# Kernel tuning notes

Hardware: AMD Instinct MI355X
Metric: run time of the kernel (lower is better)

Reference implementation:

```python
import jax, jax.numpy as jnp
import numpy as np

CHEB_K = 3

def avwgcn(x, E, w_pool, b_pool):
    # x: [B,N,C], E: [N,D], w_pool: [D,K,C,O], b_pool: [D,O]
    N = E.shape[0]
    supports = jax.nn.softmax(jax.nn.relu(E @ E.T), axis=1)  # [N,N]
    slist = [jnp.eye(N, dtype=x.dtype), supports]
    for _ in range(CHEB_K - 2):
        slist.append(2.0 * supports @ slist[-1] - slist[-2])
    S = jnp.stack(slist)                         # [K,N,N]
    W = jnp.einsum('nd,dkio->nkio', E, w_pool)   # [N,K,C,O]
    b = E @ b_pool                               # [N,O]
    xg = jnp.einsum('knm,bmc->bnkc', S, x)       # [B,N,K,C]
    return jnp.einsum('bnki,nkio->bno', xg, W) + b


def setup_inputs() -> dict:
    key = jax.random.key(0)
    ks = jax.random.split(key, 9)
    B, N, C_IN, C_OUT, D = 16, 2048, 64, 64, 10
    x = jax.random.normal(ks[0], (B, N, C_IN), dtype=jnp.float32)
    state = jax.random.normal(ks[1], (B, N, C_OUT), dtype=jnp.float32)
    node_embeddings = jax.random.normal(ks[2], (N, D), dtype=jnp.float32)
    gate_wpool = jax.random.normal(ks[3], (D, CHEB_K, C_IN + C_OUT, 2 * C_OUT), dtype=jnp.float32) * 0.1
    gate_bpool = jax.random.normal(ks[4], (D, 2 * C_OUT), dtype=jnp.float32) * 0.1
    upd_wpool = jax.random.normal(ks[5], (D, CHEB_K, C_IN + C_OUT, C_OUT), dtype=jnp.float32) * 0.1
    upd_bpool = jax.random.normal(ks[6], (D, C_OUT), dtype=jnp.float32) * 0.1
    lin_w = jax.random.normal(ks[7], (64, 128), dtype=jnp.float32) * 0.1
    lin_b = jax.random.normal(ks[8], (64,), dtype=jnp.float32) * 0.1
    return {"x": x, "state": state, "node_embeddings": node_embeddings,
            "gate_wpool": gate_wpool, "gate_bpool": gate_bpool,
            "upd_wpool": upd_wpool, "upd_bpool": upd_bpool,
            "lin_w": lin_w, "lin_b": lin_b}


def reference(x, state, node_embeddings, gate_wpool, gate_bpool, upd_wpool, upd_bpool, lin_w, lin_b):
    input_and_state = jnp.concatenate([x, state], axis=-1)          # [B,N,128]
    z_r = jax.nn.sigmoid(avwgcn(input_and_state, node_embeddings, gate_wpool, gate_bpool))  # [B,N,128]
    z_r = z_r @ lin_w.T + lin_b                                     # [B,N,64]
    candidate = jnp.concatenate([x, z_r], axis=-1)                  # [B,N,128]
    hc = jnp.tanh(avwgcn(candidate, node_embeddings, upd_wpool, upd_bpool))  # [B,N,64]
    return hc
```

## Files before the change

### kernel.cpp

```cpp
#include <hip/hip_runtime.h>

typedef unsigned short u16;
typedef short s16x8 __attribute__((ext_vector_type(8)));
typedef _Float16 h16x8 __attribute__((ext_vector_type(8)));
typedef float f32x4 __attribute__((ext_vector_type(4)));
typedef u16 u16x4 __attribute__((ext_vector_type(4)));

#define DEV static __device__ __forceinline__

DEV u16 f2h(float x){ union { _Float16 h; u16 u; } v; v.h = (_Float16)x; return v.u; }
DEV float h2f(u16 u){ union { u16 u; _Float16 h; } v; v.u = u; return (float)v.h; }
DEV void split_h(float x, u16& h, u16& l){
    h = f2h(x);
    l = f2h(x - h2f(h));
}
DEV h16x8 H8(s16x8 v){ union { s16x8 s; h16x8 h; } u; u.s = v; return u.h; }
DEV f32x4 mfma16(s16x8 a, s16x8 b, f32x4 c){
    return __builtin_amdgcn_mfma_f32_16x16x32_f16(H8(a), H8(b), c, 0, 0, 0);
}

DEV int swz(int r, int m){ return (m & ~0x38) | ((((m >> 3) ^ r) & 7) << 3); }

DEV void gll16(const u16* g, u16* l){
    __builtin_amdgcn_global_load_lds((const __attribute__((address_space(1))) void*)g,
                                     (__attribute__((address_space(3))) void*)l, 16, 0, 0);
}

__global__ __launch_bounds__(256) void k_supports(const float* __restrict__ E,
                                                  u16* __restrict__ Sh, u16* __restrict__ Sl)
{
    const int n = blockIdx.x, tid = threadIdx.x;
    const int w = tid >> 6, lane = tid & 63;
    __shared__ float red[8];

    float en[10];
    #pragma unroll
    for (int d = 0; d < 10; d++) en[d] = E[n*10 + d];

    float v[8];
    #pragma unroll
    for (int i = 0; i < 8; i++){
        int m = tid + i*256;
        const float* em = E + m*10;
        float s = 0.f;
        #pragma unroll
        for (int d = 0; d < 10; d++) s += en[d]*em[d];
        v[i] = fmaxf(s, 0.f);
    }
    float mx = v[0];
    #pragma unroll
    for (int i = 1; i < 8; i++) mx = fmaxf(mx, v[i]);
    #pragma unroll
    for (int off = 32; off > 0; off >>= 1) mx = fmaxf(mx, __shfl_xor(mx, off));
    if (lane == 0) red[w] = mx;
    __syncthreads();
    mx = fmaxf(fmaxf(red[0], red[1]), fmaxf(red[2], red[3]));
    __syncthreads();

    float sum = 0.f;
    #pragma unroll
    for (int i = 0; i < 8; i++){ v[i] = __expf(v[i] - mx); sum += v[i]; }
    #pragma unroll
    for (int off = 32; off > 0; off >>= 1) sum += __shfl_xor(sum, off);
    if (lane == 0) red[4 + w] = sum;
    __syncthreads();
    sum = red[4] + red[5] + red[6] + red[7];
    float inv = 1.f / sum;

    #pragma unroll
    for (int i = 0; i < 8; i++){
        float p = v[i] * inv;
        u16 h, l; split_h(p, h, l);
        int m = tid + i*256;
        int ms = swz(n, m);
        Sh[n*2048 + ms] = h;
        Sl[n*2048 + ms] = l;
    }
}

__global__ __launch_bounds__(256) void k_prep(const float* __restrict__ E,
    const float* __restrict__ gwp, const float* __restrict__ gbp,
    const float* __restrict__ uwp, const float* __restrict__ ubp,
    const float* __restrict__ x,   const float* __restrict__ state,
    const float* __restrict__ lw,
    u16* __restrict__ wg, u16* __restrict__ wu,
    float* __restrict__ bg, float* __restrict__ bu,
    u16* __restrict__ xt, u16* __restrict__ lwt)
{
    long idx = (long)blockIdx.x*256 + threadIdx.x;
    if (idx < 491520){
        int kk = (int)(idx & 31);
        int o  = (int)((idx >> 5) & 127);
        int r2 = (int)(idx >> 12);
        int d = r2 % 10, jc = r2 / 10;
        int j = jc*32 + kk;
        int k = j >> 7, i = j & 127;
        float v = gwp[(((d*3 + k)*128) + i)*128 + o];
        wg[idx] = f2h(v);
    } else if (idx < 737280){
        long t = idx - 491520;
        int kk = (int)(t & 31);
        int o  = (int)((t >> 5) & 63);
        int r2 = (int)(t >> 11);
        int d = r2 % 10, jc = r2 / 10;
        int j = jc*32 + kk;
        int k = j >> 7, i = j & 127;
        float v = uwp[(((d*3 + k)*128) + i)*64 + o];
        wu[t] = f2h(v);
    } else if (idx < 999424){
        long t = idx - 737280; int n = (int)(t >> 7), o = (int)(t & 127);
        float s = 0.f;
        #pragma unroll
        for (int d = 0; d < 10; d++) s += E[n*10+d]*gbp[d*128+o];
        bg[t] = s;
    } else if (idx < 1130496){
        long t = idx - 999424; int n = (int)(t >> 6), o = (int)(t & 63);
        float s = 0.f;
        #pragma unroll
        for (int d = 0; d < 10; d++) s += E[n*10+d]*ubp[d*64+o];
        bu[t] = s;
    } else if (idx < 5324800){
        long t = idx - 1130496;
        int colG = (int)(t >> 11), m = (int)(t & 2047);
        int b = colG >> 7, c = colG & 127;
        float v = (c < 64) ? x[((long)(b*2048)+m)*64 + c]
                           : state[((long)(b*2048)+m)*64 + c - 64];
        xt[(long)colG*2048 + swz(colG, m)] = f2h(v);
    } else if (idx < 5332992){
        long t = idx - 5324800;
        lwt[t] = f2h(lw[t]);
    }
}

template<int EPI>
__global__ __launch_bounds__(256) void k_gemm(
    const u16* __restrict__ Ah, const u16* __restrict__ Al,
    const u16* __restrict__ Bt,
    u16* __restrict__ Ot, float* __restrict__ Orow,
    const u16* __restrict__ Xt)
{
    __shared__ __attribute__((aligned(16))) u16 AsH[2][64*64];
    __shared__ __attribute__((aligned(16))) u16 AsL[2][64*64];
    __shared__ __attribute__((aligned(16))) u16 Bs[2][128*64];
    const int tid = threadIdx.x;
    const int xc = blockIdx.x & 7, ii = blockIdx.x >> 3;
    const int bm = ((xc & 3)*8 + (ii & 7)) << 6;
    const int bn = ((xc >> 2)*8 + (ii >> 3)) << 7;
    const int w = tid >> 6, lane = tid & 63;
    const int wm = (w & 1) << 5;
    const int wn = (w >> 1) << 6;
    const int lr = lane & 15, lk = lane >> 4;

    const int srow = tid >> 3, scol = (tid & 7) << 3;
    const long a0 = (long)(bm + srow)*2048 + scol;
    const long a1 = a0 + 32*2048;
    const long b0 = (long)(bn + srow)*2048 + scol;
    const long b1 = b0 + 32*2048;
    const long b2 = b0 + 64*2048;
    const long b3 = b0 + 96*2048;
    const int l0 = tid*8, l1 = tid*8 + 2048;

    const int c0 = (lk ^ (lr & 7)) << 3;
    const int c1 = c0 ^ 32;

#define STAGE(B, K) do { \
        gll16(Ah + a0 + (K), &AsH[B][l0]); \
        gll16(Ah + a1 + (K), &AsH[B][l1]); \
        gll16(Al + a0 + (K), &AsL[B][l0]); \
        gll16(Al + a1 + (K), &AsL[B][l1]); \
        gll16(Bt + b0 + (K), &Bs[B][l0]); \
        gll16(Bt + b1 + (K), &Bs[B][l1]); \
        gll16(Bt + b2 + (K), &Bs[B][l0 + 4096]); \
        gll16(Bt + b3 + (K), &Bs[B][l1 + 4096]); \
    } while(0)

    f32x4 acc[2][4];
    const f32x4 Z4 = {0.f, 0.f, 0.f, 0.f};
    #pragma unroll
    for (int i = 0; i < 2; i++)
        #pragma unroll
        for (int j = 0; j < 4; j++) acc[i][j] = Z4;

    STAGE(0, 0);
    __syncthreads();
    int cur = 0;
    for (int k0 = 0; k0 < 2048; k0 += 64){
        if (k0 + 64 < 2048) STAGE(cur ^ 1, k0 + 64);
        const u16* ah = AsH[cur];
        const u16* al = AsL[cur];
        const u16* bs = Bs[cur];
        #pragma unroll
        for (int s2 = 0; s2 < 2; s2++){
            const int cc = s2 ? c1 : c0;
            s16x8 bfv[4], af[2];
            #pragma unroll
            for (int ni = 0; ni < 4; ni++)
                bfv[ni] = *(const s16x8*)&bs[(wn + ni*16 + lr)*64 + cc];
            #pragma unroll
            for (int mi = 0; mi < 2; mi++)
                af[mi] = *(const s16x8*)&ah[(wm + mi*16 + lr)*64 + cc];
            #pragma unroll
            for (int mi = 0; mi < 2; mi++)
                #pragma unroll
                for (int ni = 0; ni < 4; ni++)
                    acc[mi][ni] = mfma16(af[mi], bfv[ni], acc[mi][ni]);
            #pragma unroll
            for (int mi = 0; mi < 2; mi++)
                af[mi] = *(const s16x8*)&al[(wm + mi*16 + lr)*64 + cc];
            #pragma unroll
            for (int mi = 0; mi < 2; mi++)
                #pragma unroll
                for (int ni = 0; ni < 4; ni++)
                    acc[mi][ni] = mfma16(af[mi], bfv[ni], acc[mi][ni]);
        }
        __syncthreads();
        cur ^= 1;
    }
#undef STAGE

    #pragma unroll
    for (int mi = 0; mi < 2; mi++){
        #pragma unroll
        for (int ni = 0; ni < 4; ni++){
            int i0 = bm + wm + mi*16 + lk*4;
            int j  = bn + wn + ni*16 + lr;
            f32x4 v = acc[mi][ni];
            if constexpr (EPI){
                u16x4 xh = *(const u16x4*)(Xt + (long)j*2048 + swz(j, i0));
                #pragma unroll
                for (int r = 0; r < 4; r++)
                    v[r] = 2.f*v[r] - h2f(xh[r]);
            }
            int bb = j >> 7, cc = j & 127;
            float* rp = Orow + ((long)bb*2048 + i0)*128 + cc;
            #pragma unroll
            for (int r = 0; r < 4; r++) rp[(long)r*128] = v[r];
            if constexpr (!EPI){
                u16x4 oh;
                #pragma unroll
                for (int r = 0; r < 4; r++) oh[r] = f2h(v[r]);
                *(u16x4*)(Ot + (long)j*2048 + swz(j, i0)) = oh;
            }
        }
    }
}

template<int OFULL, int ACT, int FUSE>
__global__ __launch_bounds__(256, 2) void k_combine(
    const float* __restrict__ G1r, const float* __restrict__ G2r,
    const float* __restrict__ x, const float* __restrict__ second,
    const u16* __restrict__ W,
    const float* __restrict__ bias, const float* __restrict__ E,
    float* __restrict__ out, u16* __restrict__ XtT,
    const u16* __restrict__ lwt, const float* __restrict__ lb)
{
    constexpr int NO = OFULL/32;
    __shared__ u16 Ash[64*40], Asl[64*40];
    __shared__ float Et[640];
    __shared__ u16 Zh[FUSE ? 64*136 : 1];
    __shared__ u16 Zl[FUSE ? 64*136 : 1];
    const int tid = threadIdx.x, bid = blockIdx.x;
    const int b = bid >> 5, n0 = (bid & 31) << 6;
    const int w = tid >> 6, lane = tid & 63;
    const int wm = (w & 1)*32, wo = (w >> 1)*(OFULL/2);
    const int lr = lane & 15, lk = lane >> 4;

    for (int i = tid; i < 640; i += 256)
        Et[i] = E[(n0 + (i & 63))*10 + (i >> 6)];

    const f32x4 Z4 = {0.f, 0.f, 0.f, 0.f};
    f32x4 acc[2][NO];
    #pragma unroll
    for (int mi = 0; mi < 2; mi++)
        #pragma unroll
        for (int oi = 0; oi < NO; oi++) acc[mi][oi] = Z4;

    const long rowbase = (long)b*2048 + n0;
    const int laneoff = (wo + lr)*32 + lk*8;

    s16x8 pbh[3][NO];

    for (int jc = 0; jc < 12; jc++){
        {
            const long t0 = (long)(jc*10 + 0)*OFULL*32;
            const long t1 = (long)(jc*10 + 1)*OFULL*32;
            #pragma unroll
            for (int oi = 0; oi < NO; oi++){
                pbh[0][oi] = *(const s16x8*)(W + t0 + laneoff + oi*16*32);
                pbh[1][oi] = *(const s16x8*)(W + t1 + laneoff + oi*16*32);
            }
        }
        __syncthreads();
        {
            const float* src; int stride;
            if (jc < 4){
                int col0 = jc*32;
                src = (col0 < 64) ? (x + rowbase*64 + col0)
                                  : (second + rowbase*64 + (col0 - 64));
                stride = 64;
            } else if (jc < 8){
                src = G1r + rowbase*128 + (jc-4)*32; stride = 128;
            } else {
                src = G2r + rowbase*128 + (jc-8)*32; stride = 128;
            }
            int row = tid >> 2, c8 = (tid & 3)*8;
            f32x4 s0 = *(const f32x4*)(src + (long)row*stride + c8);
            f32x4 s1 = *(const f32x4*)(src + (long)row*stride + c8 + 4);
            s16x8 vh, vl;
            #pragma unroll
            for (int t = 0; t < 4; t++){
                u16 h,l; split_h(s0[t], h, l); vh[t]=(short)h; vl[t]=(short)l;
            }
            #pragma unroll
            for (int t = 0; t < 4; t++){
                u16 h,l; split_h(s1[t], h, l); vh[4+t]=(short)h; vl[4+t]=(short)l;
            }
            *(s16x8*)&Ash[row*40 + c8] = vh;
            *(s16x8*)&Asl[row*40 + c8] = vl;
        }
        __syncthreads();

        s16x8 ah[2], al[2];
        #pragma unroll
        for (int mi = 0; mi < 2; mi++){
            ah[mi] = *(const s16x8*)&Ash[(wm + mi*16 + lr)*40 + lk*8];
            al[mi] = *(const s16x8*)&Asl[(wm + mi*16 + lr)*40 + lk*8];
        }

        #pragma unroll
        for (int d = 0; d < 10; d++){
            const int cur = d % 3;
            if (d < 8){
                const int nx = (d + 2) % 3;
                const long t2 = (long)(jc*10 + d + 2)*OFULL*32;
                #pragma unroll
                for (int oi = 0; oi < NO; oi++)
                    pbh[nx][oi] = *(const s16x8*)(W + t2 + laneoff + oi*16*32);
            }
            f32x4 Cd[2][NO];
            #pragma unroll
            for (int mi = 0; mi < 2; mi++)
                #pragma unroll
                for (int oi = 0; oi < NO; oi++)
                    Cd[mi][oi] = mfma16(ah[mi], pbh[cur][oi], Z4);
            #pragma unroll
            for (int mi = 0; mi < 2; mi++)
                #pragma unroll
                for (int oi = 0; oi < NO; oi++)
                    Cd[mi][oi] = mfma16(al[mi], pbh[cur][oi], Cd[mi][oi]);
            #pragma unroll
            for (int mi = 0; mi < 2; mi++){
                f32x4 e4 = *(const f32x4*)&Et[d*64 + wm + mi*16 + lk*4];
                #pragma unroll
                for (int oi = 0; oi < NO; oi++) acc[mi][oi] += e4 * Cd[mi][oi];
            }
        }
    }

    if constexpr (!FUSE){
        #pragma unroll
        for (int mi = 0; mi < 2; mi++){
            #pragma unroll
            for (int oi = 0; oi < NO; oi++){
                int mrow = n0 + wm + mi*16 + lk*4;
                int o = wo + oi*16 + lr;
                #pragma unroll
                for (int r = 0; r < 4; r++){
                    float v = acc[mi][oi][r] + bias[(long)(mrow + r)*OFULL + o];
                    v = (ACT == 0) ? (1.f/(1.f + __expf(-v))) : tanhf(v);
                    out[((long)b*2048 + mrow + r)*OFULL + o] = v;
                }
            }
        }
    } else {
        #pragma unroll
        for (int mi = 0; mi < 2; mi++){
            #pragma unroll
            for (int oi = 0; oi < NO; oi++){
                int lrow = wm + mi*16 + lk*4;
                int o = wo + oi*16 + lr;
                #pragma unroll
                for (int r = 0; r < 4; r++){
                    float v = acc[mi][oi][r] + bias[(long)(n0 + lrow + r)*OFULL + o];
                    v = 1.f/(1.f + __expf(-v));
                    u16 h, l; split_h(v, h, l);
                    Zh[(lrow + r)*136 + o] = h;
                    Zl[(lrow + r)*136 + o] = l;
                }
            }
        }
        __syncthreads();
        f32x4 az[4];
        #pragma unroll
        for (int mi = 0; mi < 4; mi++) az[mi] = Z4;
        const int oz = w*16 + lr;
        #pragma unroll
        for (int ks = 0; ks < 4; ks++){
            s16x8 bw = *(const s16x8*)(lwt + oz*128 + ks*32 + lk*8);
            #pragma unroll
            for (int mi = 0; mi < 4; mi++){
                s16x8 zh = *(const s16x8*)&Zh[(mi*16 + lr)*136 + ks*32 + lk*8];
                az[mi] = mfma16(zh, bw, az[mi]);
            }
            #pragma unroll
            for (int mi = 0; mi < 4; mi++){
                s16x8 zl = *(const s16x8*)&Zl[(mi*16 + lr)*136 + ks*32 + lk*8];
                az[mi] = mfma16(zl, bw, az[mi]);
            }
        }
        const float lbv = lb[w*16 + lr];
        const int colG = b*128 + 64 + w*16 + lr;
        #pragma unroll
        for (int mi = 0; mi < 4; mi++){
            int mrow = n0 + mi*16 + lk*4;
            u16x4 tq;
            #pragma unroll
            for (int r = 0; r < 4; r++){
                float v = az[mi][r] + lbv;
                out[((long)b*2048 + mrow + r)*64 + w*16 + lr] = v;
                tq[r] = f2h(v);
            }
            *(u16x4*)(XtT + (long)colG*2048 + swz(colG, mrow)) = tq;
        }
    }
}

extern "C" void kernel_launch(void* const* d_in, const int* in_sizes, int n_in,
                              void* d_out, int out_size, void* d_ws, size_t ws_size,
                              hipStream_t stream)
{
    const float* x   = (const float*)d_in[0];
    const float* st  = (const float*)d_in[1];
    const float* E   = (const float*)d_in[2];
    const float* gwp = (const float*)d_in[3];
    const float* gbp = (const float*)d_in[4];
    const float* uwp = (const float*)d_in[5];
    const float* ubp = (const float*)d_in[6];
    const float* lw  = (const float*)d_in[7];
    const float* lb  = (const float*)d_in[8];
    float* out = (float*)d_out;
    char* ws = (char*)d_ws;

    const size_t MB8 = 8388608;
    u16*   Sh   = (u16*)(ws);
    u16*   Sl   = (u16*)(ws + 1*MB8);
    u16*   Xt   = (u16*)(ws + 2*MB8);
    u16*   G1t  = (u16*)(ws + 3*MB8);
    float* G1row= (float*)(ws + 4*MB8);
    float* G2row= (float*)(ws + 6*MB8);
    float* zr   = (float*)(ws + 8*MB8);
    char*  p    = ws + 9*MB8;
    u16* wg = (u16*)p;             p += 983040;
    u16* wu = (u16*)p;             p += 491520;
    float* bg = (float*)p;         p += 1048576;
    float* bu = (float*)p;         p += 524288;
    u16* lwt = (u16*)p;            p += 16384;

    k_supports<<<dim3(2048), dim3(256), 0, stream>>>(E, Sh, Sl);
    k_prep<<<dim3(20832), dim3(256), 0, stream>>>(E, gwp, gbp, uwp, ubp, x, st, lw,
                                                  wg, wu, bg, bu, Xt, lwt);
    k_gemm<0><<<dim3(512), dim3(256), 0, stream>>>(Sh, Sl, Xt, G1t, G1row,
                                                   (const u16*)nullptr);
    k_gemm<1><<<dim3(512), dim3(256), 0, stream>>>(Sh, Sl, G1t, (u16*)nullptr, G2row,
                                                   Xt);
    k_combine<128,0,1><<<dim3(512), dim3(256), 0, stream>>>(G1row, G2row, x, st,
                                                            wg, bg, E, zr, Xt, lwt, lb);
    k_gemm<0><<<dim3(512), dim3(256), 0, stream>>>(Sh, Sl, Xt, G1t, G1row,
                                                   (const u16*)nullptr);
    k_gemm<1><<<dim3(512), dim3(256), 0, stream>>>(Sh, Sl, G1t, (u16*)nullptr, G2row,
                                                   Xt);
    k_combine<64,1,0><<<dim3(512), dim3(256), 0, stream>>>(G1row, G2row, x, zr,
                                                           wu, bu, E, out,
                                                           (u16*)nullptr,
                                                           (const u16*)nullptr,
                                                           (const float*)nullptr);
}
```

Before: 357.3 us.

## Switch GEMM to 32x32x16 MFMA and fold supports kernel into prep

Replaces the 16x16x32 MFMA tiling in the propagation GEMM with 32x32x16 MFMAs: each wave now computes two 32x32 tiles, with the LDS fragment addressing and epilogue register mapping rewritten to match. This cuts the number of LDS fragment reads per MFMA and the instruction count. Separately, the softmax-supports kernel is merged into the prep kernel as its first 2048 blocks, saving one launch. The new swizzled read index and output mapping must line up exactly with the existing swizzle, which is a correctness risk.

```diff
diff --git a/kernel.cpp b/kernel.cpp
--- a/kernel.cpp
+++ b/kernel.cpp
@@ -4,6 +4,7 @@
 typedef short s16x8 __attribute__((ext_vector_type(8)));
 typedef _Float16 h16x8 __attribute__((ext_vector_type(8)));
 typedef float f32x4 __attribute__((ext_vector_type(4)));
+typedef float f32x16 __attribute__((ext_vector_type(16)));
 typedef u16 u16x4 __attribute__((ext_vector_type(4)));
 
 #define DEV static __device__ __forceinline__
@@ -18,64 +19,15 @@
 DEV f32x4 mfma16(s16x8 a, s16x8 b, f32x4 c){
     return __builtin_amdgcn_mfma_f32_16x16x32_f16(H8(a), H8(b), c, 0, 0, 0);
 }
+DEV f32x16 mfma32(s16x8 a, s16x8 b, f32x16 c){
+    return __builtin_amdgcn_mfma_f32_32x32x16_f16(H8(a), H8(b), c, 0, 0, 0);
+}
 
 DEV int swz(int r, int m){ return (m & ~0x38) | ((((m >> 3) ^ r) & 7) << 3); }
 
 DEV void gll16(const u16* g, u16* l){
     __builtin_amdgcn_global_load_lds((const __attribute__((address_space(1))) void*)g,
                                      (__attribute__((address_space(3))) void*)l, 16, 0, 0);
-}
-
-__global__ __launch_bounds__(256) void k_supports(const float* __restrict__ E,
-                                                  u16* __restrict__ Sh, u16* __restrict__ Sl)
-{
-    const int n = blockIdx.x, tid = threadIdx.x;
-    const int w = tid >> 6, lane = tid & 63;
-    __shared__ float red[8];
-
-    float en[10];
-    #pragma unroll
-    for (int d = 0; d < 10; d++) en[d] = E[n*10 + d];
-
-    float v[8];
-    #pragma unroll
-    for (int i = 0; i < 8; i++){
-        int m = tid + i*256;
-        const float* em = E + m*10;
-        float s = 0.f;
-        #pragma unroll
-        for (int d = 0; d < 10; d++) s += en[d]*em[d];
-        v[i] = fmaxf(s, 0.f);
-    }
-    float mx = v[0];
-    #pragma unroll
-    for (int i = 1; i < 8; i++) mx = fmaxf(mx, v[i]);
-    #pragma unroll
-    for (int off = 32; off > 0; off >>= 1) mx = fmaxf(mx, __shfl_xor(mx, off));
-    if (lane == 0) red[w] = mx;
-    __syncthreads();
-    mx = fmaxf(fmaxf(red[0], red[1]), fmaxf(red[2], red[3]));
-    __syncthreads();
-
-    float sum = 0.f;
-    #pragma unroll
-    for (int i = 0; i < 8; i++){ v[i] = __expf(v[i] - mx); sum += v[i]; }
-    #pragma unroll
-    for (int off = 32; off > 0; off >>= 1) sum += __shfl_xor(sum, off);
-    if (lane == 0) red[4 + w] = sum;
-    __syncthreads();
-    sum = red[4] + red[5] + red[6] + red[7];
-    float inv = 1.f / sum;
-
-    #pragma unroll
-    for (int i = 0; i < 8; i++){
-        float p = v[i] * inv;
-        u16 h, l; split_h(p, h, l);
-        int m = tid + i*256;
-        int ms = swz(n, m);
-        Sh[n*2048 + ms] = h;
-        Sl[n*2048 + ms] = l;
-    }
 }
 
 __global__ __launch_bounds__(256) void k_prep(const float* __restrict__ E,
@@ -85,9 +37,56 @@
     const float* __restrict__ lw,
     u16* __restrict__ wg, u16* __restrict__ wu,
     float* __restrict__ bg, float* __restrict__ bu,
-    u16* __restrict__ xt, u16* __restrict__ lwt)
+    u16* __restrict__ xt, u16* __restrict__ lwt,
+    u16* __restrict__ Sh, u16* __restrict__ Sl)
 {
-    long idx = (long)blockIdx.x*256 + threadIdx.x;
+    __shared__ float red[8];
+    const int tid = threadIdx.x;
+    if (blockIdx.x < 2048){
+        const int n = blockIdx.x;
+        const int w = tid >> 6, lane = tid & 63;
+        float en[10];
+        #pragma unroll
+        for (int d = 0; d < 10; d++) en[d] = E[n*10 + d];
+        float v[8];
+        #pragma unroll
+        for (int i = 0; i < 8; i++){
+            int m = tid + i*256;
+            const float* em = E + m*10;
+            float s = 0.f;
+            #pragma unroll
+            for (int d = 0; d < 10; d++) s += en[d]*em[d];
+            v[i] = fmaxf(s, 0.f);
+        }
+        float mx = v[0];
+        #pragma unroll
+        for (int i = 1; i < 8; i++) mx = fmaxf(mx, v[i]);
+        #pragma unroll
+        for (int off = 32; off > 0; off >>= 1) mx = fmaxf(mx, __shfl_xor(mx, off));
+        if (lane == 0) red[w] = mx;
+        __syncthreads();
+        mx = fmaxf(fmaxf(red[0], red[1]), fmaxf(red[2], red[3]));
+        __syncthreads();
+        float sum = 0.f;
+        #pragma unroll
+        for (int i = 0; i < 8; i++){ v[i] = __expf(v[i] - mx); sum += v[i]; }
+        #pragma unroll
+        for (int off = 32; off > 0; off >>= 1) sum += __shfl_xor(sum, off);
+        if (lane == 0) red[4 + w] = sum;
+        __syncthreads();
+        sum = red[4] + red[5] + red[6] + red[7];
+        float inv = 1.f / sum;
+        #pragma unroll
+        for (int i = 0; i < 8; i++){
+            float p = v[i] * inv;
+            u16 h, l; split_h(p, h, l);
+            int ms = swz(n, tid + i*256);
+            Sh[n*2048 + ms] = h;
+            Sl[n*2048 + ms] = l;
+        }
+        return;
+    }
+    long idx = (long)(blockIdx.x - 2048)*256 + tid;
     if (idx < 491520){
         int kk = (int)(idx & 31);
         int o  = (int)((idx >> 5) & 127);
@@ -149,7 +148,9 @@
     const int w = tid >> 6, lane = tid & 63;
     const int wm = (w & 1) << 5;
     const int wn = (w >> 1) << 6;
-    const int lr = lane & 15, lk = lane >> 4;
+    const int r31 = lane & 31;
+    const int hk  = lane >> 5;
+    const int key = lane & 7;
 
     const int srow = tid >> 3, scol = (tid & 7) << 3;
     const long a0 = (long)(bm + srow)*2048 + scol;
@@ -159,9 +160,6 @@
     const long b2 = b0 + 64*2048;
     const long b3 = b0 + 96*2048;
     const int l0 = tid*8, l1 = tid*8 + 2048;
-
-    const int c0 = (lk ^ (lr & 7)) << 3;
-    const int c1 = c0 ^ 32;
 
 #define STAGE(B, K) do { \
         gll16(Ah + a0 + (K), &AsH[B][l0]); \
@@ -174,12 +172,11 @@
         gll16(Bt + b3 + (K), &Bs[B][l1 + 4096]); \
     } while(0)
 
-    f32x4 acc[2][4];
-    const f32x4 Z4 = {0.f, 0.f, 0.f, 0.f};
+    f32x16 acc[2];
     #pragma unroll
     for (int i = 0; i < 2; i++)
         #pragma unroll
-        for (int j = 0; j < 4; j++) acc[i][j] = Z4;
+        for (int r = 0; r < 16; r++) acc[i][r] = 0.f;
 
     STAGE(0, 0);
     __syncthreads();
@@ -190,28 +187,16 @@
         const u16* al = AsL[cur];
         const u16* bs = Bs[cur];
         #pragma unroll
-        for (int s2 = 0; s2 < 2; s2++){
-            const int cc = s2 ? c1 : c0;
-            s16x8 bfv[4], af[2];
-            #pragma unroll
-            for (int ni = 0; ni < 4; ni++)
-                bfv[ni] = *(const s16x8*)&bs[(wn + ni*16 + lr)*64 + cc];
-            #pragma unroll
-            for (int mi = 0; mi < 2; mi++)
-                af[mi] = *(const s16x8*)&ah[(wm + mi*16 + lr)*64 + cc];
-            #pragma unroll
-            for (int mi = 0; mi < 2; mi++)
-                #pragma unroll
-                for (int ni = 0; ni < 4; ni++)
-                    acc[mi][ni] = mfma16(af[mi], bfv[ni], acc[mi][ni]);
-            #pragma unroll
-            for (int mi = 0; mi < 2; mi++)
-                af[mi] = *(const s16x8*)&al[(wm + mi*16 + lr)*64 + cc];
-            #pragma unroll
-            for (int mi = 0; mi < 2; mi++)
-                #pragma unroll
-                for (int ni = 0; ni < 4; ni++)
-                    acc[mi][ni] = mfma16(af[mi], bfv[ni], acc[mi][ni]);
+        for (int ks = 0; ks < 4; ks++){
+            const int ca = (((2*ks + hk) ^ key)) << 3;
+            s16x8 bv0 = *(const s16x8*)&bs[(wn +  0 + r31)*64 + ca];
+            s16x8 bv1 = *(const s16x8*)&bs[(wn + 32 + r31)*64 + ca];
+            s16x8 avh = *(const s16x8*)&ah[(wm + r31)*64 + ca];
+            acc[0] = mfma32(avh, bv0, acc[0]);
+            acc[1] = mfma32(avh, bv1, acc[1]);
+            s16x8 avl = *(const s16x8*)&al[(wm + r31)*64 + ca];
+            acc[0] = mfma32(avl, bv0, acc[0]);
+            acc[1] = mfma32(avl, bv1, acc[1]);
         }
         __syncthreads();
         cur ^= 1;
@@ -219,26 +204,28 @@
 #undef STAGE
 
     #pragma unroll
-    for (int mi = 0; mi < 2; mi++){
-        #pragma unroll
-        for (int ni = 0; ni < 4; ni++){
-            int i0 = bm + wm + mi*16 + lk*4;
-            int j  = bn + wn + ni*16 + lr;
-            f32x4 v = acc[mi][ni];
+    for (int ni = 0; ni < 2; ni++){
+        int j  = bn + wn + ni*32 + r31;
+        int bb = j >> 7, cc = j & 127;
+        #pragma unroll
+        for (int g = 0; g < 4; g++){
+            int i0 = bm + wm + 4*hk + 8*g;
+            f32x4 v;
+            #pragma unroll
+            for (int q = 0; q < 4; q++) v[q] = acc[ni][4*g + q];
             if constexpr (EPI){
                 u16x4 xh = *(const u16x4*)(Xt + (long)j*2048 + swz(j, i0));
                 #pragma unroll
-                for (int r = 0; r < 4; r++)
-                    v[r] = 2.f*v[r] - h2f(xh[r]);
-            }
-            int bb = j >> 7, cc = j & 127;
+                for (int q = 0; q < 4; q++)
+                    v[q] = 2.f*v[q] - h2f(xh[q]);
+            }
             float* rp = Orow + ((long)bb*2048 + i0)*128 + cc;
             #pragma unroll
-            for (int r = 0; r < 4; r++) rp[(long)r*128] = v[r];
+            for (int q = 0; q < 4; q++) rp[(long)q*128] = v[q];
             if constexpr (!EPI){
                 u16x4 oh;
                 #pragma unroll
-                for (int r = 0; r < 4; r++) oh[r] = f2h(v[r]);
+                for (int q = 0; q < 4; q++) oh[q] = f2h(v[q]);
                 *(u16x4*)(Ot + (long)j*2048 + swz(j, i0)) = oh;
             }
         }
@@ -456,9 +443,8 @@
     float* bu = (float*)p;         p += 524288;
     u16* lwt = (u16*)p;            p += 16384;
 
-    k_supports<<<dim3(2048), dim3(256), 0, stream>>>(E, Sh, Sl);
-    k_prep<<<dim3(20832), dim3(256), 0, stream>>>(E, gwp, gbp, uwp, ubp, x, st, lw,
-                                                  wg, wu, bg, bu, Xt, lwt);
+    k_prep<<<dim3(22880), dim3(256), 0, stream>>>(E, gwp, gbp, uwp, ubp, x, st, lw,
+                                                  wg, wu, bg, bu, Xt, lwt, Sh, Sl);
     k_gemm<0><<<dim3(512), dim3(256), 0, stream>>>(Sh, Sl, Xt, G1t, G1row,
                                                    (const u16*)nullptr);
     k_gemm<1><<<dim3(512), dim3(256), 0, stream>>>(Sh, Sl, G1t, (u16*)nullptr, G2row,
```

Result: slower. 374.1 us (+4.7%).

## Merge supports into prep kernel and widen gate combine to 512 threads

Applied to the files above, without the earlier changes.

The softmax-supports kernel is folded into the prep kernel as its first 2048 blocks, which removes one launch and lets the two independent pieces of work overlap. The gate combine kernel becomes a dedicated 512-thread version in which each of eight waves owns 16 output columns across all 64 rows, so per-thread register pressure drops and more waves are available to hide latency. The fused z_r linear stage is split across the eight waves by rows and columns. The cost is more redundant A-tile fragment loads per wave and different occupancy behaviour at the larger block size.

```diff
diff --git a/kernel.cpp b/kernel.cpp
--- a/kernel.cpp
+++ b/kernel.cpp
@@ -24,58 +24,6 @@
 DEV void gll16(const u16* g, u16* l){
     __builtin_amdgcn_global_load_lds((const __attribute__((address_space(1))) void*)g,
                                      (__attribute__((address_space(3))) void*)l, 16, 0, 0);
-}
-
-__global__ __launch_bounds__(256) void k_supports(const float* __restrict__ E,
-                                                  u16* __restrict__ Sh, u16* __restrict__ Sl)
-{
-    const int n = blockIdx.x, tid = threadIdx.x;
-    const int w = tid >> 6, lane = tid & 63;
-    __shared__ float red[8];
-
-    float en[10];
-    #pragma unroll
-    for (int d = 0; d < 10; d++) en[d] = E[n*10 + d];
-
-    float v[8];
-    #pragma unroll
-    for (int i = 0; i < 8; i++){
-        int m = tid + i*256;
-        const float* em = E + m*10;
-        float s = 0.f;
-        #pragma unroll
-        for (int d = 0; d < 10; d++) s += en[d]*em[d];
-        v[i] = fmaxf(s, 0.f);
-    }
-    float mx = v[0];
-    #pragma unroll
-    for (int i = 1; i < 8; i++) mx = fmaxf(mx, v[i]);
-    #pragma unroll
-    for (int off = 32; off > 0; off >>= 1) mx = fmaxf(mx, __shfl_xor(mx, off));
-    if (lane == 0) red[w] = mx;
-    __syncthreads();
-    mx = fmaxf(fmaxf(red[0], red[1]), fmaxf(red[2], red[3]));
-    __syncthreads();
-
-    float sum = 0.f;
-    #pragma unroll
-    for (int i = 0; i < 8; i++){ v[i] = __expf(v[i] - mx); sum += v[i]; }
-    #pragma unroll
-    for (int off = 32; off > 0; off >>= 1) sum += __shfl_xor(sum, off);
-    if (lane == 0) red[4 + w] = sum;
-    __syncthreads();
-    sum = red[4] + red[5] + red[6] + red[7];
-    float inv = 1.f / sum;
-
-    #pragma unroll
-    for (int i = 0; i < 8; i++){
-        float p = v[i] * inv;
-        u16 h, l; split_h(p, h, l);
-        int m = tid + i*256;
-        int ms = swz(n, m);
-        Sh[n*2048 + ms] = h;
-        Sl[n*2048 + ms] = l;
-    }
 }
 
 __global__ __launch_bounds__(256) void k_prep(const float* __restrict__ E,
@@ -85,9 +33,56 @@
     const float* __restrict__ lw,
     u16* __restrict__ wg, u16* __restrict__ wu,
     float* __restrict__ bg, float* __restrict__ bu,
-    u16* __restrict__ xt, u16* __restrict__ lwt)
+    u16* __restrict__ xt, u16* __restrict__ lwt,
+    u16* __restrict__ Sh, u16* __restrict__ Sl)
 {
-    long idx = (long)blockIdx.x*256 + threadIdx.x;
+    __shared__ float red[8];
+    const int tid = threadIdx.x;
+    if (blockIdx.x < 2048){
+        const int n = blockIdx.x;
+        const int w = tid >> 6, lane = tid & 63;
+        float en[10];
+        #pragma unroll
+        for (int d = 0; d < 10; d++) en[d] = E[n*10 + d];
+        float v[8];
+        #pragma unroll
+        for (int i = 0; i < 8; i++){
+            int m = tid + i*256;
+            const float* em = E + m*10;
+            float s = 0.f;
+            #pragma unroll
+            for (int d = 0; d < 10; d++) s += en[d]*em[d];
+            v[i] = fmaxf(s, 0.f);
+        }
+        float mx = v[0];
+        #pragma unroll
+        for (int i = 1; i < 8; i++) mx = fmaxf(mx, v[i]);
+        #pragma unroll
+        for (int off = 32; off > 0; off >>= 1) mx = fmaxf(mx, __shfl_xor(mx, off));
+        if (lane == 0) red[w] = mx;
+        __syncthreads();
+        mx = fmaxf(fmaxf(red[0], red[1]), fmaxf(red[2], red[3]));
+        __syncthreads();
+        float sum = 0.f;
+        #pragma unroll
+        for (int i = 0; i < 8; i++){ v[i] = __expf(v[i] - mx); sum += v[i]; }
+        #pragma unroll
+        for (int off = 32; off > 0; off >>= 1) sum += __shfl_xor(sum, off);
+        if (lane == 0) red[4 + w] = sum;
+        __syncthreads();
+        sum = red[4] + red[5] + red[6] + red[7];
+        float inv = 1.f / sum;
+        #pragma unroll
+        for (int i = 0; i < 8; i++){
+            float p = v[i] * inv;
+            u16 h, l; split_h(p, h, l);
+            int ms = swz(n, tid + i*256);
+            Sh[n*2048 + ms] = h;
+            Sl[n*2048 + ms] = l;
+        }
+        return;
+    }
+    long idx = (long)(blockIdx.x - 2048)*256 + tid;
     if (idx < 491520){
         int kk = (int)(idx & 31);
         int o  = (int)((idx >> 5) & 127);
@@ -245,8 +240,7 @@
     }
 }
 
-template<int OFULL, int ACT, int FUSE>
-__global__ __launch_bounds__(256, 2) void k_combine(
+__global__ __launch_bounds__(512) void k_combineG(
     const float* __restrict__ G1r, const float* __restrict__ G2r,
     const float* __restrict__ x, const float* __restrict__ second,
     const u16* __restrict__ W,
@@ -254,41 +248,34 @@
     float* __restrict__ out, u16* __restrict__ XtT,
     const u16* __restrict__ lwt, const float* __restrict__ lb)
 {
-    constexpr int NO = OFULL/32;
     __shared__ u16 Ash[64*40], Asl[64*40];
     __shared__ float Et[640];
-    __shared__ u16 Zh[FUSE ? 64*136 : 1];
-    __shared__ u16 Zl[FUSE ? 64*136 : 1];
+    __shared__ u16 Zh[64*136], Zl[64*136];
     const int tid = threadIdx.x, bid = blockIdx.x;
     const int b = bid >> 5, n0 = (bid & 31) << 6;
     const int w = tid >> 6, lane = tid & 63;
-    const int wm = (w & 1)*32, wo = (w >> 1)*(OFULL/2);
+    const int wo = w << 4;
     const int lr = lane & 15, lk = lane >> 4;
 
-    for (int i = tid; i < 640; i += 256)
+    for (int i = tid; i < 640; i += 512)
         Et[i] = E[(n0 + (i & 63))*10 + (i >> 6)];
 
     const f32x4 Z4 = {0.f, 0.f, 0.f, 0.f};
-    f32x4 acc[2][NO];
-    #pragma unroll
-    for (int mi = 0; mi < 2; mi++)
-        #pragma unroll
-        for (int oi = 0; oi < NO; oi++) acc[mi][oi] = Z4;
+    f32x4 acc[4];
+    #pragma unroll
+    for (int mi = 0; mi < 4; mi++) acc[mi] = Z4;
 
     const long rowbase = (long)b*2048 + n0;
     const int laneoff = (wo + lr)*32 + lk*8;
 
-    s16x8 pbh[3][NO];
+    s16x8 pbh[3];
 
     for (int jc = 0; jc < 12; jc++){
         {
-            const long t0 = (long)(jc*10 + 0)*OFULL*32;
-            const long t1 = (long)(jc*10 + 1)*OFULL*32;
-            #pragma unroll
-            for (int oi = 0; oi < NO; oi++){
-                pbh[0][oi] = *(const s16x8*)(W + t0 + laneoff + oi*16*32);
-                pbh[1][oi] = *(const s16x8*)(W + t1 + laneoff + oi*16*32);
-            }
+            const long t0 = (long)(jc*10 + 0)*128*32;
+            const long t1 = (long)(jc*10 + 1)*128*32;
+            pbh[0] = *(const s16x8*)(W + t0 + laneoff);
+            pbh[1] = *(const s16x8*)(W + t1 + laneoff);
         }
         __syncthreads();
         {
@@ -303,6 +290,150 @@
             } else {
                 src = G2r + rowbase*128 + (jc-8)*32; stride = 128;
             }
+            int row = tid >> 3, c4 = (tid & 7)*4;
+            f32x4 s0 = *(const f32x4*)(src + (long)row*stride + c4);
+            u16x4 vh, vl;
+            #pragma unroll
+            for (int t = 0; t < 4; t++){
+                u16 h,l; split_h(s0[t], h, l); vh[t]=h; vl[t]=l;
+            }
+            *(u16x4*)&Ash[row*40 + c4] = vh;
+            *(u16x4*)&Asl[row*40 + c4] = vl;
+        }
+        __syncthreads();
+
+        s16x8 ah[4], al[4];
+        #pragma unroll
+        for (int mi = 0; mi < 4; mi++){
+            ah[mi] = *(const s16x8*)&Ash[(mi*16 + lr)*40 + lk*8];
+            al[mi] = *(const s16x8*)&Asl[(mi*16 + lr)*40 + lk*8];
+        }
+
+        #pragma unroll
+        for (int d = 0; d < 10; d++){
+            const int cur = d % 3;
+            if (d < 8){
+                const int nx = (d + 2) % 3;
+                const long t2 = (long)(jc*10 + d + 2)*128*32;
+                pbh[nx] = *(const s16x8*)(W + t2 + laneoff);
+            }
+            f32x4 Cd[4];
+            #pragma unroll
+            for (int mi = 0; mi < 4; mi++)
+                Cd[mi] = mfma16(ah[mi], pbh[cur], Z4);
+            #pragma unroll
+            for (int mi = 0; mi < 4; mi++)
+                Cd[mi] = mfma16(al[mi], pbh[cur], Cd[mi]);
+            #pragma unroll
+            for (int mi = 0; mi < 4; mi++){
+                f32x4 e4 = *(const f32x4*)&Et[d*64 + mi*16 + lk*4];
+                acc[mi] += e4 * Cd[mi];
+            }
+        }
+    }
+
+    #pragma unroll
+    for (int mi = 0; mi < 4; mi++){
+        int lrow = mi*16 + lk*4;
+        int o = wo + lr;
+        #pragma unroll
+        for (int r = 0; r < 4; r++){
+            float v = acc[mi][r] + bias[(long)(n0 + lrow + r)*128 + o];
+            v = 1.f/(1.f + __expf(-v));
+            u16 h, l; split_h(v, h, l);
+            Zh[(lrow + r)*136 + o] = h;
+            Zl[(lrow + r)*136 + o] = l;
+        }
+    }
+    __syncthreads();
+    f32x4 az[2] = {Z4, Z4};
+    const int ow = (w & 3) << 4;
+    const int rh = (w >> 2) << 5;
+    #pragma unroll
+    for (int ks = 0; ks < 4; ks++){
+        s16x8 bw = *(const s16x8*)(lwt + (ow + lr)*128 + ks*32 + lk*8);
+        #pragma unroll
+        for (int mi = 0; mi < 2; mi++){
+            s16x8 zh = *(const s16x8*)&Zh[(rh + mi*16 + lr)*136 + ks*32 + lk*8];
+            az[mi] = mfma16(zh, bw, az[mi]);
+        }
+        #pragma unroll
+        for (int mi = 0; mi < 2; mi++){
+            s16x8 zl = *(const s16x8*)&Zl[(rh + mi*16 + lr)*136 + ks*32 + lk*8];
+            az[mi] = mfma16(zl, bw, az[mi]);
+        }
+    }
+    const float lbv = lb[ow + lr];
+    const int colG = b*128 + 64 + ow + lr;
+    #pragma unroll
+    for (int mi = 0; mi < 2; mi++){
+        int mrow = n0 + rh + mi*16 + lk*4;
+        u16x4 tq;
+        #pragma unroll
+        for (int r = 0; r < 4; r++){
+            float v = az[mi][r] + lbv;
+            out[((long)b*2048 + mrow + r)*64 + ow + lr] = v;
+            tq[r] = f2h(v);
+        }
+        *(u16x4*)(XtT + (long)colG*2048 + swz(colG, mrow)) = tq;
+    }
+}
+
+template<int OFULL, int ACT>
+__global__ __launch_bounds__(256, 2) void k_combine(
+    const float* __restrict__ G1r, const float* __restrict__ G2r,
+    const float* __restrict__ x, const float* __restrict__ second,
+    const u16* __restrict__ W,
+    const float* __restrict__ bias, const float* __restrict__ E,
+    float* __restrict__ out)
+{
+    constexpr int NO = OFULL/32;
+    __shared__ u16 Ash[64*40], Asl[64*40];
+    __shared__ float Et[640];
+    const int tid = threadIdx.x, bid = blockIdx.x;
+    const int b = bid >> 5, n0 = (bid & 31) << 6;
+    const int w = tid >> 6, lane = tid & 63;
+    const int wm = (w & 1)*32, wo = (w >> 1)*(OFULL/2);
+    const int lr = lane & 15, lk = lane >> 4;
+
+    for (int i = tid; i < 640; i += 256)
+        Et[i] = E[(n0 + (i & 63))*10 + (i >> 6)];
+
+    const f32x4 Z4 = {0.f, 0.f, 0.f, 0.f};
+    f32x4 acc[2][NO];
+    #pragma unroll
+    for (int mi = 0; mi < 2; mi++)
+        #pragma unroll
+        for (int oi = 0; oi < NO; oi++) acc[mi][oi] = Z4;
+
+    const long rowbase = (long)b*2048 + n0;
+    const int laneoff = (wo + lr)*32 + lk*8;
+
+    s16x8 pbh[3][NO];
+
+    for (int jc = 0; jc < 12; jc++){
+        {
+            const long t0 = (long)(jc*10 + 0)*OFULL*32;
+            const long t1 = (long)(jc*10 + 1)*OFULL*32;
+            #pragma unroll
+            for (int oi = 0; oi < NO; oi++){
+                pbh[0][oi] = *(const s16x8*)(W + t0 + laneoff + oi*16*32);
+                pbh[1][oi] = *(const s16x8*)(W + t1 + laneoff + oi*16*32);
+            }
+        }
+        __syncthreads();
+        {
+            const float* src; int stride;
+            if (jc < 4){
+                int col0 = jc*32;
+                src = (col0 < 64) ? (x + rowbase*64 + col0)
+                                  : (second + rowbase*64 + (col0 - 64));
+                stride = 64;
+            } else if (jc < 8){
+                src = G1r + rowbase*128 + (jc-4)*32; stride = 128;
+            } else {
+                src = G2r + rowbase*128 + (jc-8)*32; stride = 128;
+            }
             int row = tid >> 2, c8 = (tid & 3)*8;
             f32x4 s0 = *(const f32x4*)(src + (long)row*stride + c8);
             f32x4 s1 = *(const f32x4*)(src + (long)row*stride + c8 + 4);
@@ -357,70 +488,18 @@
         }
     }
 
-    if constexpr (!FUSE){
-        #pragma unroll
-        for (int mi = 0; mi < 2; mi++){
-            #pragma unroll
-            for (int oi = 0; oi < NO; oi++){
-                int mrow = n0 + wm + mi*16 + lk*4;
-                int o = wo + oi*16 + lr;
-                #pragma unroll
-                for (int r = 0; r < 4; r++){
-                    float v = acc[mi][oi][r] + bias[(long)(mrow + r)*OFULL + o];
-                    v = (ACT == 0) ? (1.f/(1.f + __expf(-v))) : tanhf(v);
-                    out[((long)b*2048 + mrow + r)*OFULL + o] = v;
-                }
-            }
-        }
-    } else {
-        #pragma unroll
-        for (int mi = 0; mi < 2; mi++){
-            #pragma unroll
-            for (int oi = 0; oi < NO; oi++){
-                int lrow = wm + mi*16 + lk*4;
-                int o = wo + oi*16 + lr;
-                #pragma unroll
-                for (int r = 0; r < 4; r++){
-                    float v = acc[mi][oi][r] + bias[(long)(n0 + lrow + r)*OFULL + o];
-                    v = 1.f/(1.f + __expf(-v));
-                    u16 h, l; split_h(v, h, l);
-                    Zh[(lrow + r)*136 + o] = h;
-                    Zl[(lrow + r)*136 + o] = l;
-                }
-            }
-        }
-        __syncthreads();
-        f32x4 az[4];
-        #pragma unroll
-        for (int mi = 0; mi < 4; mi++) az[mi] = Z4;
-        const int oz = w*16 + lr;
-        #pragma unroll
-        for (int ks = 0; ks < 4; ks++){
-            s16x8 bw = *(const s16x8*)(lwt + oz*128 + ks*32 + lk*8);
-            #pragma unroll
-            for (int mi = 0; mi < 4; mi++){
-                s16x8 zh = *(const s16x8*)&Zh[(mi*16 + lr)*136 + ks*32 + lk*8];
-                az[mi] = mfma16(zh, bw, az[mi]);
-            }
-            #pragma unroll
-            for (int mi = 0; mi < 4; mi++){
-                s16x8 zl = *(const s16x8*)&Zl[(mi*16 + lr)*136 + ks*32 + lk*8];
-                az[mi] = mfma16(zl, bw, az[mi]);
-            }
-        }
-        const float lbv = lb[w*16 + lr];
-        const int colG = b*128 + 64 + w*16 + lr;
-        #pragma unroll
-        for (int mi = 0; mi < 4; mi++){
-            int mrow = n0 + mi*16 + lk*4;
-            u16x4 tq;
+    #pragma unroll
+    for (int mi = 0; mi < 2; mi++){
+        #pragma unroll
+        for (int oi = 0; oi < NO; oi++){
+            int mrow = n0 + wm + mi*16 + lk*4;
+            int o = wo + oi*16 + lr;
             #pragma unroll
             for (int r = 0; r < 4; r++){
-                float v = az[mi][r] + lbv;
-                out[((long)b*2048 + mrow + r)*64 + w*16 + lr] = v;
-                tq[r] = f2h(v);
-            }
-            *(u16x4*)(XtT + (long)colG*2048 + swz(colG, mrow)) = tq;
+                float v = acc[mi][oi][r] + bias[(long)(mrow + r)*OFULL + o];
+                v = (ACT == 0) ? (1.f/(1.f + __expf(-v))) : tanhf(v);
+                out[((long)b*2048 + mrow + r)*OFULL + o] = v;
+            }
         }
     }
 }
@@ -456,22 +535,18 @@
     float* bu = (float*)p;         p += 524288;
     u16* lwt = (u16*)p;            p += 16384;
 
-    k_supports<<<dim3(2048), dim3(256), 0, stream>>>(E, Sh, Sl);
-    k_prep<<<dim3(20832), dim3(256), 0, stream>>>(E, gwp, gbp, uwp, ubp, x, st, lw,
-                                                  wg, wu, bg, bu, Xt, lwt);
+    k_prep<<<dim3(22880), dim3(256), 0, stream>>>(E, gwp, gbp, uwp, ubp, x, st, lw,
+                                                  wg, wu, bg, bu, Xt, lwt, Sh, Sl);
     k_gemm<0><<<dim3(512), dim3(256), 0, stream>>>(Sh, Sl, Xt, G1t, G1row,
                                                    (const u16*)nullptr);
     k_gemm<1><<<dim3(512), dim3(256), 0, stream>>>(Sh, Sl, G1t, (u16*)nullptr, G2row,
                                                    Xt);
-    k_combine<128,0,1><<<dim3(512), dim3(256), 0, stream>>>(G1row, G2row, x, st,
-                                                            wg, bg, E, zr, Xt, lwt, lb);
+    k_combineG<<<dim3(512), dim3(512), 0, stream>>>(G1row, G2row, x, st,
+                                                    wg, bg, E, zr, Xt, lwt, lb);
     k_gemm<0><<<dim3(512), dim3(256), 0, stream>>>(Sh, Sl, Xt, G1t, G1row,
                                                    (const u16*)nullptr);
     k_gemm<1><<<dim3(512), dim3(256), 0, stream>>>(Sh, Sl, G1t, (u16*)nullptr, G2row,
                                                    Xt);
-    k_combine<64,1,0><<<dim3(512), dim3(256), 0, stream>>>(G1row, G2row, x, zr,
-                                                           wu, bu, E, out,
-                                                           (u16*)nullptr,
-                                                           (const u16*)nullptr,
-                                                           (const float*)nullptr);
-}
+    k_combine<64,1><<<dim3(512), dim3(256), 0, stream>>>(G1row, G2row, x, zr,
+                                                         wu, bu, E, out);
+}
```

Measured after the change: 353.7 us. About the same (-1.0%).
